# Performance work log

Hardware: AMD Instinct MI355X
Metric: run time of the kernel (lower is better)

The kernel has to match this reference:

```python
import jax, jax.numpy as jnp
import numpy as np

NHEAD = 16
THETA = 10000.0


def _rope_cos_sin(seq_len, head_dim, dtype=jnp.float32):
    # matches precompute_freqs_cis: freqs over even indices, outer with positions
    inv = 1.0 / (THETA ** (jnp.arange(0, head_dim, 2, dtype=jnp.float32) / head_dim))  # [hd/2]
    ang = jnp.arange(seq_len, dtype=jnp.float32)[:, None] * inv[None, :]  # [S, hd/2]
    return jnp.cos(ang).astype(dtype), jnp.sin(ang).astype(dtype)


def _apply_rope(x, cos, sin):
    # x: [B, S, H, D]; pairs (even, odd) treated as complex, multiplied by cis
    B, S, H, D = x.shape
    xr = x.reshape(B, S, H, D // 2, 2)
    a, b = xr[..., 0], xr[..., 1]
    c = cos[None, :, None, :]
    s = sin[None, :, None, :]
    out = jnp.stack([a * c - b * s, a * s + b * c], axis=-1)
    return out.reshape(B, S, H, D)


def setup_inputs() -> dict:
    key = jax.random.key(0)
    ks = jax.random.split(key, 9)
    B, S, D, A = 4, 2048, 1024, 1024
    w = lambda k, i, o: jax.random.normal(k, (i, o), jnp.float32) * 0.02
    return {
        "x": jax.random.normal(ks[0], (B, S, D), jnp.float32),
        "Wq": w(ks[1], D, A), "bq": jnp.zeros((A,), jnp.float32),
        "Wk": w(ks[2], D, A), "bk": jnp.zeros((A,), jnp.float32),
        "Wv": w(ks[3], D, A), "bv": jnp.zeros((A,), jnp.float32),
        "Wo": w(ks[4], A, D), "bo": jnp.zeros((D,), jnp.float32),
    }


def reference(x, Wq, bq, Wk, bk, Wv, bv, Wo, bo):
    B, S, D = x.shape
    A = Wq.shape[1]
    hd = A // NHEAD
    scale = 1.0 / np.sqrt(A / NHEAD)  # 1/dk with dk = sqrt(att_model/nhead)

    Q = (x @ Wq + bq).reshape(B, S, NHEAD, hd)
    K = (x @ Wk + bk).reshape(B, S, NHEAD, hd)
    V = (x @ Wv + bv).reshape(B, S, NHEAD, hd)

    cos, sin = _rope_cos_sin(S, hd)
    Q = _apply_rope(Q, cos, sin)
    K = _apply_rope(K, cos, sin)

    # [B, H, S, S] scores (module materializes this unfused)
    scores = jnp.einsum("bqhd,bkhd->bhqk", Q, K) * scale
    attn = jax.nn.softmax(scores, axis=-1)
    out = jnp.einsum("bhqk,bkhd->bqhd", attn, V).reshape(B, S, A)
    return out @ Wo + bo
```

## Files before the change

### kernel.cpp

```cpp
#include <hip/hip_runtime.h>
#include <math.h>

#define B_N 4
#define S_N 2048
#define D_N 1024
#define H_N 16
#define HD_N 64
#define M_N (B_N * S_N)

typedef __attribute__((ext_vector_type(8))) short bf16x8;
typedef __attribute__((ext_vector_type(4))) float f32x4;

static __device__ __forceinline__ unsigned short f2bf(float f) {
    unsigned int u = __float_as_uint(f);
    u += 0x7FFF + ((u >> 16) & 1);
    return (unsigned short)(u >> 16);
}
static __device__ __forceinline__ float bf2f(unsigned short h) {
    return __uint_as_float(((unsigned int)h) << 16);
}

__global__ __launch_bounds__(256)
void rope_table_kernel(float* __restrict__ cos_t, float* __restrict__ sin_t) {
    int idx = blockIdx.x * 256 + threadIdx.x;
    if (idx >= S_N * 32) return;
    int sp = idx >> 5;
    int p  = idx & 31;
    float inv = powf(10000.0f, -(float)p / 32.0f);
    float ang = (float)sp * inv;
    float s, c;
    sincosf(ang, &s, &c);
    cos_t[idx] = c;
    sin_t[idx] = s;
}

__global__ __launch_bounds__(256)
void splitT_w_kernel(const float* __restrict__ W0, const float* __restrict__ W1,
                     const float* __restrict__ W2, const float* __restrict__ W3,
                     unsigned short* __restrict__ WTh, unsigned short* __restrict__ WTl)
{
    __shared__ float tile[64][65];
    const int k0  = blockIdx.x * 64;
    const int n0  = blockIdx.y * 64;
    const int mat = blockIdx.z;
    const float* __restrict__ W = (mat == 0) ? W0 : (mat == 1) ? W1 : (mat == 2) ? W2 : W3;
    const int t = threadIdx.x;

    #pragma unroll
    for (int p = 0; p < 4; ++p) {
        int idx = t + p * 256;
        int r = idx >> 4, c4 = (idx & 15) * 4;
        float4 v = *(const float4*)&W[(size_t)(k0 + r) * D_N + n0 + c4];
        tile[r][c4]     = v.x;
        tile[r][c4 + 1] = v.y;
        tile[r][c4 + 2] = v.z;
        tile[r][c4 + 3] = v.w;
    }
    __syncthreads();
    #pragma unroll
    for (int p = 0; p < 4; ++p) {
        int idx = t + p * 256;
        int nl = idx >> 4, kc = (idx & 15) * 4;
        ushort4 hi, lo;
        float f0 = tile[kc][nl], f1 = tile[kc + 1][nl];
        float f2 = tile[kc + 2][nl], f3 = tile[kc + 3][nl];
        hi.x = f2bf(f0); lo.x = f2bf(f0 - bf2f(hi.x));
        hi.y = f2bf(f1); lo.y = f2bf(f1 - bf2f(hi.y));
        hi.z = f2bf(f2); lo.z = f2bf(f2 - bf2f(hi.z));
        hi.w = f2bf(f3); lo.w = f2bf(f3 - bf2f(hi.w));
        size_t base = ((size_t)(mat * D_N + n0 + nl)) * D_N + k0 + kc;
        *(ushort4*)&WTh[base] = hi;
        *(ushort4*)&WTl[base] = lo;
    }
}

__device__ __forceinline__ void gemm_core_f32A(
    const float* __restrict__ A,
    const unsigned short* __restrict__ Bh, const unsigned short* __restrict__ Bl,
    int aRow0, int bRow0,
    unsigned short* ldsA, unsigned short* ldsB,
    f32x4 acc[4][4])
{
    const int tid  = threadIdx.x;
    const int wave = tid >> 6;
    const int lane = tid & 63;
    const int l15  = lane & 15;
    const int lg   = lane >> 4;
    const int wr   = wave >> 1;
    const int wc   = wave & 1;

    const float* ga[2];
    int la[2];
    #pragma unroll
    for (int p = 0; p < 2; ++p) {
        int c = tid + p * 256;
        int row = c >> 2, kc = c & 3;
        ga[p] = A + (size_t)(aRow0 + row) * D_N + kc * 8;
        la[p] = row * 72 + kc * 8;
    }
    const unsigned short* gb[4];
    int lb[4];
    #pragma unroll
    for (int p = 0; p < 4; ++p) {
        int c = tid + p * 256;
        int row = c >> 3, ss = c & 7, sel = ss >> 2, kc = ss & 3;
        gb[p] = (sel ? Bl : Bh) + (size_t)(bRow0 + row) * D_N + kc * 8;
        lb[p] = row * 72 + ss * 8;
    }

    for (int kk = 0; kk < D_N / 32; ++kk) {
        float4 av[2][2];
        bf16x8 bv[4];
        #pragma unroll
        for (int p = 0; p < 2; ++p) {
            av[p][0] = *(const float4*)ga[p];
            av[p][1] = *(const float4*)(ga[p] + 4);
            ga[p] += 32;
        }
        #pragma unroll
        for (int p = 0; p < 4; ++p) {
            bv[p] = *(const bf16x8*)gb[p];
            gb[p] += 32;
        }
        __syncthreads();
        #pragma unroll
        for (int p = 0; p < 2; ++p) {
            bf16x8 hi, lo;
            float v[8] = {av[p][0].x, av[p][0].y, av[p][0].z, av[p][0].w,
                          av[p][1].x, av[p][1].y, av[p][1].z, av[p][1].w};
            #pragma unroll
            for (int q = 0; q < 8; ++q) {
                unsigned short h = f2bf(v[q]);
                hi[q] = (short)h;
                lo[q] = (short)f2bf(v[q] - bf2f(h));
            }
            *(bf16x8*)&ldsA[la[p]]      = hi;
            *(bf16x8*)&ldsA[la[p] + 32] = lo;
        }
        #pragma unroll
        for (int p = 0; p < 4; ++p)
            *(bf16x8*)&ldsB[lb[p]] = bv[p];
        __syncthreads();

        bf16x8 ah[4], al[4], bh[4], bl[4];
        #pragma unroll
        for (int i = 0; i < 4; ++i) {
            int ar = wr * 64 + i * 16 + l15;
            ah[i] = *(const bf16x8*)&ldsA[ar * 72 + lg * 8];
            al[i] = *(const bf16x8*)&ldsA[ar * 72 + 32 + lg * 8];
            int br = wc * 64 + i * 16 + l15;
            bh[i] = *(const bf16x8*)&ldsB[br * 72 + lg * 8];
            bl[i] = *(const bf16x8*)&ldsB[br * 72 + 32 + lg * 8];
        }
        #pragma unroll
        for (int i = 0; i < 4; ++i)
            #pragma unroll
            for (int j = 0; j < 4; ++j) {
                acc[i][j] = __builtin_amdgcn_mfma_f32_16x16x32_bf16(ah[i], bh[j], acc[i][j], 0, 0, 0);
                acc[i][j] = __builtin_amdgcn_mfma_f32_16x16x32_bf16(al[i], bh[j], acc[i][j], 0, 0, 0);
                acc[i][j] = __builtin_amdgcn_mfma_f32_16x16x32_bf16(ah[i], bl[j], acc[i][j], 0, 0, 0);
            }
    }
}

__global__ __launch_bounds__(256)
void qkv_gemm_kernel(const float* __restrict__ x,
                     const unsigned short* __restrict__ WTh, const unsigned short* __restrict__ WTl,
                     const float* __restrict__ bq, const float* __restrict__ bk,
                     const float* __restrict__ bv_,
                     const float* __restrict__ cos_t, const float* __restrict__ sin_t,
                     unsigned short* __restrict__ Qh, unsigned short* __restrict__ Ql,
                     unsigned short* __restrict__ Kh, unsigned short* __restrict__ Kl,
                     unsigned short* __restrict__ Vth, unsigned short* __restrict__ Vtl)
{
    __shared__ unsigned short ldsA[128 * 72];
    __shared__ unsigned short ldsB[128 * 72];

    const int m0  = blockIdx.x * 128;
    const int n0  = blockIdx.y * 128;
    const int mat = n0 >> 10;

    f32x4 acc[4][4];
    #pragma unroll
    for (int i = 0; i < 4; ++i)
        #pragma unroll
        for (int j = 0; j < 4; ++j) acc[i][j] = (f32x4){0.f, 0.f, 0.f, 0.f};

    gemm_core_f32A(x, WTh, WTl, m0, n0, ldsA, ldsB, acc);

    const int tid  = threadIdx.x;
    const int wave = tid >> 6;
    const int lane = tid & 63;
    const int l15  = lane & 15;
    const int lg   = lane >> 4;
    const int wr   = wave >> 1;
    const int wc   = wave & 1;

    const float* __restrict__ bias = (mat == 0) ? bq : (mat == 1) ? bk : bv_;
    unsigned short* __restrict__ Hi = (mat == 0) ? Qh : Kh;
    unsigned short* __restrict__ Lo = (mat == 0) ? Ql : Kl;

    #pragma unroll
    for (int i = 0; i < 4; ++i) {
        #pragma unroll
        for (int j = 0; j < 4; ++j) {
            const int nl   = (n0 & 1023) + wc * 64 + j * 16 + l15;
            const int head = nl >> 6;
            const int d    = nl & 63;
            const float bval = bias[nl];
            const int m_base = m0 + wr * 64 + i * 16 + lg * 4;
            const int bb  = m_base >> 11;
            const int sp0 = m_base & (S_N - 1);

            if (mat == 2) {
                ushort4 hi4, lo4;
                float v0 = acc[i][j][0] + bval;
                float v1 = acc[i][j][1] + bval;
                float v2 = acc[i][j][2] + bval;
                float v3 = acc[i][j][3] + bval;
                hi4.x = f2bf(v0); lo4.x = f2bf(v0 - bf2f(hi4.x));
                hi4.y = f2bf(v1); lo4.y = f2bf(v1 - bf2f(hi4.y));
                hi4.z = f2bf(v2); lo4.z = f2bf(v2 - bf2f(hi4.z));
                hi4.w = f2bf(v3); lo4.w = f2bf(v3 - bf2f(hi4.w));
                size_t base = ((size_t)((bb * H_N + head) * HD_N + d)) * S_N + sp0;
                *(ushort4*)&Vth[base] = hi4;
                *(ushort4*)&Vtl[base] = lo4;
            } else {
                const int p = d >> 1;
                const float sgn = (d & 1) ? 1.0f : -1.0f;
                #pragma unroll
                for (int r = 0; r < 4; ++r) {
                    int sp = sp0 + r;
                    float v = acc[i][j][r] + bval;
                    float part = __shfl_xor(v, 1);
                    float c = cos_t[sp * 32 + p];
                    float s = sin_t[sp * 32 + p];
                    float vp = v * c + part * s * sgn;
                    if (mat == 0) vp *= 0.125f;
                    unsigned short hi = f2bf(vp);
                    unsigned short lo = f2bf(vp - bf2f(hi));
                    size_t base = ((size_t)((bb * H_N + head) * S_N + sp)) * HD_N + d;
                    Hi[base] = hi;
                    Lo[base] = lo;
                }
            }
        }
    }
}

__global__ __launch_bounds__(256)
void attn_kernel(const unsigned short* __restrict__ Qh, const unsigned short* __restrict__ Ql,
                 const unsigned short* __restrict__ Kh, const unsigned short* __restrict__ Kl,
                 const unsigned short* __restrict__ Vh, const unsigned short* __restrict__ Vl,
                 float* __restrict__ O)
{
    __shared__ __align__(16) unsigned short KhS[4096];
    __shared__ __align__(16) unsigned short KlS[4096];
    __shared__ __align__(16) unsigned short VhS[4096];
    __shared__ __align__(16) unsigned short VlS[4096];
    __shared__ __align__(16) unsigned short Pb[4][1024];

    const int qt = blockIdx.x;
    const int h  = blockIdx.y;
    const int b  = blockIdx.z;
    const int bh = b * H_N + h;

    const int tid  = threadIdx.x;
    const int wave = tid >> 6;
    const int lane = tid & 63;
    const int l15  = lane & 15;
    const int lg   = lane >> 4;

    const int qrow = qt * 64 + wave * 16 + l15;
    const size_t qbase = ((size_t)bh * S_N + qrow) * HD_N;
    bf16x8 qfh[2], qfl[2];
    qfh[0] = *(const bf16x8*)&Qh[qbase + lg * 8];
    qfh[1] = *(const bf16x8*)&Qh[qbase + 32 + lg * 8];
    qfl[0] = *(const bf16x8*)&Ql[qbase + lg * 8];
    qfl[1] = *(const bf16x8*)&Ql[qbase + 32 + lg * 8];

    f32x4 oacc[4];
    #pragma unroll
    for (int dt = 0; dt < 4; ++dt) oacc[dt] = (f32x4){0.f, 0.f, 0.f, 0.f};
    float m_r[4], l_r[4];
    #pragma unroll
    for (int r = 0; r < 4; ++r) { m_r[r] = -1e30f; l_r[r] = 0.f; }

    for (int kt = 0; kt < S_N / 64; ++kt) {
        __syncthreads();
        #pragma unroll
        for (int t = 0; t < 2; ++t) {
            int c   = tid + t * 256;
            int row = c >> 3;
            int sl  = c & 7;
            int li  = (row * 64 + sl * 8) ^ ((row & 7) << 3);
            size_t gk = ((size_t)bh * S_N + kt * 64 + row) * HD_N + sl * 8;
            size_t gv = ((size_t)bh * HD_N + row) * S_N + kt * 64 + sl * 8;
            bf16x8 vkh = *(const bf16x8*)&Kh[gk];
            bf16x8 vkl = *(const bf16x8*)&Kl[gk];
            bf16x8 vvh = *(const bf16x8*)&Vh[gv];
            bf16x8 vvl = *(const bf16x8*)&Vl[gv];
            *(bf16x8*)&KhS[li] = vkh;
            *(bf16x8*)&KlS[li] = vkl;
            *(bf16x8*)&VhS[li] = vvh;
            *(bf16x8*)&VlS[li] = vvl;
        }
        __syncthreads();

        f32x4 s[4];
        #pragma unroll
        for (int nt = 0; nt < 4; ++nt) s[nt] = (f32x4){0.f, 0.f, 0.f, 0.f};
        #pragma unroll
        for (int ks = 0; ks < 2; ++ks) {
            #pragma unroll
            for (int nt = 0; nt < 4; ++nt) {
                int row = nt * 16 + l15;
                int bi  = (row * 64 + ks * 32 + lg * 8) ^ ((row & 7) << 3);
                bf16x8 fkh = *(const bf16x8*)&KhS[bi];
                bf16x8 fkl = *(const bf16x8*)&KlS[bi];
                s[nt] = __builtin_amdgcn_mfma_f32_16x16x32_bf16(qfh[ks], fkh, s[nt], 0, 0, 0);
                s[nt] = __builtin_amdgcn_mfma_f32_16x16x32_bf16(qfl[ks], fkh, s[nt], 0, 0, 0);
                s[nt] = __builtin_amdgcn_mfma_f32_16x16x32_bf16(qfh[ks], fkl, s[nt], 0, 0, 0);
            }
        }

        #pragma unroll
        for (int r = 0; r < 4; ++r) {
            float mx = fmaxf(fmaxf(s[0][r], s[1][r]), fmaxf(s[2][r], s[3][r]));
            mx = fmaxf(mx, __shfl_xor(mx, 1));
            mx = fmaxf(mx, __shfl_xor(mx, 2));
            mx = fmaxf(mx, __shfl_xor(mx, 4));
            mx = fmaxf(mx, __shfl_xor(mx, 8));
            float mnew = fmaxf(m_r[r], mx);
            float al   = __expf(m_r[r] - mnew);
            float ps   = 0.f;
            #pragma unroll
            for (int nt = 0; nt < 4; ++nt) {
                float p = __expf(s[nt][r] - mnew);
                s[nt][r] = p;
                ps += p;
            }
            ps += __shfl_xor(ps, 1);
            ps += __shfl_xor(ps, 2);
            ps += __shfl_xor(ps, 4);
            ps += __shfl_xor(ps, 8);
            l_r[r] = l_r[r] * al + ps;
            m_r[r] = mnew;
            oacc[0][r] *= al; oacc[1][r] *= al;
            oacc[2][r] *= al; oacc[3][r] *= al;
            int prow = lg * 4 + r;
            #pragma unroll
            for (int nt = 0; nt < 4; ++nt) {
                Pb[wave][(prow * 64 + nt * 16 + l15) ^ ((prow & 7) << 3)] = f2bf(s[nt][r]);
            }
        }
        asm volatile("s_waitcnt lgkmcnt(0)" ::: "memory");

        #pragma unroll
        for (int ks = 0; ks < 2; ++ks) {
            int pi = (l15 * 64 + ks * 32 + lg * 8) ^ ((l15 & 7) << 3);
            bf16x8 pa = *(const bf16x8*)&Pb[wave][pi];
            #pragma unroll
            for (int dt = 0; dt < 4; ++dt) {
                int vrow = dt * 16 + l15;
                int vbi  = (vrow * 64 + ks * 32 + lg * 8) ^ ((vrow & 7) << 3);
                bf16x8 fvh = *(const bf16x8*)&VhS[vbi];
                bf16x8 fvl = *(const bf16x8*)&VlS[vbi];
                oacc[dt] = __builtin_amdgcn_mfma_f32_16x16x32_bf16(pa, fvh, oacc[dt], 0, 0, 0);
                oacc[dt] = __builtin_amdgcn_mfma_f32_16x16x32_bf16(pa, fvl, oacc[dt], 0, 0, 0);
            }
        }
    }

    #pragma unroll
    for (int r = 0; r < 4; ++r) {
        float inv = 1.0f / l_r[r];
        int row = qt * 64 + wave * 16 + lg * 4 + r;
        size_t obase = ((size_t)b * S_N + row) * D_N + h * HD_N;
        #pragma unroll
        for (int dt = 0; dt < 4; ++dt)
            O[obase + dt * 16 + l15] = oacc[dt][r] * inv;
    }
}

__global__ __launch_bounds__(256)
void out_gemm_kernel(const float* __restrict__ A,
                     const unsigned short* __restrict__ WTh, const unsigned short* __restrict__ WTl,
                     const float* __restrict__ bo, float* __restrict__ out)
{
    __shared__ unsigned short ldsA[128 * 72];
    __shared__ unsigned short ldsB[128 * 72];

    const int m0 = blockIdx.x * 128;
    const int n0 = blockIdx.y * 128;

    f32x4 acc[4][4];
    #pragma unroll
    for (int i = 0; i < 4; ++i)
        #pragma unroll
        for (int j = 0; j < 4; ++j) acc[i][j] = (f32x4){0.f, 0.f, 0.f, 0.f};

    gemm_core_f32A(A, WTh, WTl, m0, 3 * D_N + n0, ldsA, ldsB, acc);

    const int tid  = threadIdx.x;
    const int wave = tid >> 6;
    const int lane = tid & 63;
    const int l15  = lane & 15;
    const int lg   = lane >> 4;
    const int wr   = wave >> 1;
    const int wc   = wave & 1;

    #pragma unroll
    for (int i = 0; i < 4; ++i) {
        #pragma unroll
        for (int j = 0; j < 4; ++j) {
            int n = n0 + wc * 64 + j * 16 + l15;
            float bval = bo[n];
            int m_base = m0 + wr * 64 + i * 16 + lg * 4;
            #pragma unroll
            for (int r = 0; r < 4; ++r)
                out[(size_t)(m_base + r) * D_N + n] = acc[i][j][r] + bval;
        }
    }
}

extern "C" void kernel_launch(void* const* d_in, const int* in_sizes, int n_in,
                              void* d_out, int out_size, void* d_ws, size_t ws_size,
                              hipStream_t stream) {
    const float* x  = (const float*)d_in[0];
    const float* Wq = (const float*)d_in[1];
    const float* bq = (const float*)d_in[2];
    const float* Wk = (const float*)d_in[3];
    const float* bk = (const float*)d_in[4];
    const float* Wv = (const float*)d_in[5];
    const float* bv = (const float*)d_in[6];
    const float* Wo = (const float*)d_in[7];
    const float* bo = (const float*)d_in[8];
    float* out = (float*)d_out;

    const size_t NE = (size_t)B_N * H_N * S_N * HD_N;
    const size_t WTE = (size_t)4 * D_N * D_N;

    float* cos_t = (float*)d_ws;
    float* sin_t = cos_t + (size_t)S_N * 32;
    unsigned short* WTh = (unsigned short*)(sin_t + (size_t)S_N * 32);
    unsigned short* WTl = WTh + WTE;
    unsigned short* Qh  = WTl + WTE;
    unsigned short* Ql  = Qh  + NE;
    unsigned short* Kh  = Ql  + NE;
    unsigned short* Kl  = Kh  + NE;
    unsigned short* Vth = Kl  + NE;
    unsigned short* Vtl = Vth + NE;
    float* Obuf = (float*)(Vtl + NE);

    rope_table_kernel<<<256, 256, 0, stream>>>(cos_t, sin_t);

    dim3 gw(16, 16, 4);
    splitT_w_kernel<<<gw, 256, 0, stream>>>(Wq, Wk, Wv, Wo, WTh, WTl);

    dim3 g1(M_N / 128, 24);
    qkv_gemm_kernel<<<g1, 256, 0, stream>>>(x, WTh, WTl, bq, bk, bv,
                                            cos_t, sin_t,
                                            Qh, Ql, Kh, Kl, Vth, Vtl);

    dim3 g2(S_N / 64, H_N, B_N);
    attn_kernel<<<g2, 256, 0, stream>>>(Qh, Ql, Kh, Kl, Vth, Vtl, Obuf);

    dim3 g3(M_N / 128, 8);
    out_gemm_kernel<<<g3, 256, 0, stream>>>(Obuf, WTh, WTl, bo, out);
}
```

Before: 661.6 us.

## Process two query row blocks per wave in attention to reuse K/V tiles

```diff
diff --git a/kernel.cpp b/kernel.cpp
--- a/kernel.cpp
+++ b/kernel.cpp
@@ -258,7 +258,7 @@
     __shared__ __align__(16) unsigned short KlS[4096];
     __shared__ __align__(16) unsigned short VhS[4096];
     __shared__ __align__(16) unsigned short VlS[4096];
-    __shared__ __align__(16) unsigned short Pb[4][1024];
+    __shared__ __align__(16) unsigned short Pb[4][2048];
 
     const int qt = blockIdx.x;
     const int h  = blockIdx.y;
@@ -271,20 +271,26 @@
     const int l15  = lane & 15;
     const int lg   = lane >> 4;
 
-    const int qrow = qt * 64 + wave * 16 + l15;
-    const size_t qbase = ((size_t)bh * S_N + qrow) * HD_N;
-    bf16x8 qfh[2], qfl[2];
-    qfh[0] = *(const bf16x8*)&Qh[qbase + lg * 8];
-    qfh[1] = *(const bf16x8*)&Qh[qbase + 32 + lg * 8];
-    qfl[0] = *(const bf16x8*)&Ql[qbase + lg * 8];
-    qfl[1] = *(const bf16x8*)&Ql[qbase + 32 + lg * 8];
-
-    f32x4 oacc[4];
-    #pragma unroll
-    for (int dt = 0; dt < 4; ++dt) oacc[dt] = (f32x4){0.f, 0.f, 0.f, 0.f};
-    float m_r[4], l_r[4];
-    #pragma unroll
-    for (int r = 0; r < 4; ++r) { m_r[r] = -1e30f; l_r[r] = 0.f; }
+    bf16x8 qfh[2][2], qfl[2][2];
+    #pragma unroll
+    for (int rb = 0; rb < 2; ++rb) {
+        const int qrow = qt * 128 + wave * 32 + rb * 16 + l15;
+        const size_t qbase = ((size_t)bh * S_N + qrow) * HD_N;
+        qfh[rb][0] = *(const bf16x8*)&Qh[qbase + lg * 8];
+        qfh[rb][1] = *(const bf16x8*)&Qh[qbase + 32 + lg * 8];
+        qfl[rb][0] = *(const bf16x8*)&Ql[qbase + lg * 8];
+        qfl[rb][1] = *(const bf16x8*)&Ql[qbase + 32 + lg * 8];
+    }
+
+    f32x4 oacc[2][4];
+    float m_r[2][4], l_r[2][4];
+    #pragma unroll
+    for (int rb = 0; rb < 2; ++rb) {
+        #pragma unroll
+        for (int dt = 0; dt < 4; ++dt) oacc[rb][dt] = (f32x4){0.f, 0.f, 0.f, 0.f};
+        #pragma unroll
+        for (int r = 0; r < 4; ++r) { m_r[rb][r] = -1e30f; l_r[rb][r] = 0.f; }
+    }
 
     for (int kt = 0; kt < S_N / 64; ++kt) {
         __syncthreads();
@@ -307,9 +313,12 @@
         }
         __syncthreads();
 
-        f32x4 s[4];
-        #pragma unroll
-        for (int nt = 0; nt < 4; ++nt) s[nt] = (f32x4){0.f, 0.f, 0.f, 0.f};
+        f32x4 s[2][4];
+        #pragma unroll
+        for (int rb = 0; rb < 2; ++rb)
+            #pragma unroll
+            for (int nt = 0; nt < 4; ++nt) s[rb][nt] = (f32x4){0.f, 0.f, 0.f, 0.f};
+        __builtin_amdgcn_s_setprio(1);
         #pragma unroll
         for (int ks = 0; ks < 2; ++ks) {
             #pragma unroll
@@ -318,68 +327,84 @@
                 int bi  = (row * 64 + ks * 32 + lg * 8) ^ ((row & 7) << 3);
                 bf16x8 fkh = *(const bf16x8*)&KhS[bi];
                 bf16x8 fkl = *(const bf16x8*)&KlS[bi];
-                s[nt] = __builtin_amdgcn_mfma_f32_16x16x32_bf16(qfh[ks], fkh, s[nt], 0, 0, 0);
-                s[nt] = __builtin_amdgcn_mfma_f32_16x16x32_bf16(qfl[ks], fkh, s[nt], 0, 0, 0);
-                s[nt] = __builtin_amdgcn_mfma_f32_16x16x32_bf16(qfh[ks], fkl, s[nt], 0, 0, 0);
-            }
-        }
-
-        #pragma unroll
-        for (int r = 0; r < 4; ++r) {
-            float mx = fmaxf(fmaxf(s[0][r], s[1][r]), fmaxf(s[2][r], s[3][r]));
-            mx = fmaxf(mx, __shfl_xor(mx, 1));
-            mx = fmaxf(mx, __shfl_xor(mx, 2));
-            mx = fmaxf(mx, __shfl_xor(mx, 4));
-            mx = fmaxf(mx, __shfl_xor(mx, 8));
-            float mnew = fmaxf(m_r[r], mx);
-            float al   = __expf(m_r[r] - mnew);
-            float ps   = 0.f;
-            #pragma unroll
-            for (int nt = 0; nt < 4; ++nt) {
-                float p = __expf(s[nt][r] - mnew);
-                s[nt][r] = p;
-                ps += p;
-            }
-            ps += __shfl_xor(ps, 1);
-            ps += __shfl_xor(ps, 2);
-            ps += __shfl_xor(ps, 4);
-            ps += __shfl_xor(ps, 8);
-            l_r[r] = l_r[r] * al + ps;
-            m_r[r] = mnew;
-            oacc[0][r] *= al; oacc[1][r] *= al;
-            oacc[2][r] *= al; oacc[3][r] *= al;
-            int prow = lg * 4 + r;
-            #pragma unroll
-            for (int nt = 0; nt < 4; ++nt) {
-                Pb[wave][(prow * 64 + nt * 16 + l15) ^ ((prow & 7) << 3)] = f2bf(s[nt][r]);
+                #pragma unroll
+                for (int rb = 0; rb < 2; ++rb) {
+                    s[rb][nt] = __builtin_amdgcn_mfma_f32_16x16x32_bf16(qfh[rb][ks], fkh, s[rb][nt], 0, 0, 0);
+                    s[rb][nt] = __builtin_amdgcn_mfma_f32_16x16x32_bf16(qfl[rb][ks], fkh, s[rb][nt], 0, 0, 0);
+                    s[rb][nt] = __builtin_amdgcn_mfma_f32_16x16x32_bf16(qfh[rb][ks], fkl, s[rb][nt], 0, 0, 0);
+                }
+            }
+        }
+        __builtin_amdgcn_s_setprio(0);
+
+        #pragma unroll
+        for (int rb = 0; rb < 2; ++rb) {
+            #pragma unroll
+            for (int r = 0; r < 4; ++r) {
+                float mx = fmaxf(fmaxf(s[rb][0][r], s[rb][1][r]), fmaxf(s[rb][2][r], s[rb][3][r]));
+                mx = fmaxf(mx, __shfl_xor(mx, 1));
+                mx = fmaxf(mx, __shfl_xor(mx, 2));
+                mx = fmaxf(mx, __shfl_xor(mx, 4));
+                mx = fmaxf(mx, __shfl_xor(mx, 8));
+                float mnew = fmaxf(m_r[rb][r], mx);
+                float al   = __expf(m_r[rb][r] - mnew);
+                float ps   = 0.f;
+                #pragma unroll
+                for (int nt = 0; nt < 4; ++nt) {
+                    float p = __expf(s[rb][nt][r] - mnew);
+                    s[rb][nt][r] = p;
+                    ps += p;
+                }
+                ps += __shfl_xor(ps, 1);
+                ps += __shfl_xor(ps, 2);
+                ps += __shfl_xor(ps, 4);
+                ps += __shfl_xor(ps, 8);
+                l_r[rb][r] = l_r[rb][r] * al + ps;
+                m_r[rb][r] = mnew;
+                oacc[rb][0][r] *= al; oacc[rb][1][r] *= al;
+                oacc[rb][2][r] *= al; oacc[rb][3][r] *= al;
+                int prow = rb * 16 + lg * 4 + r;
+                #pragma unroll
+                for (int nt = 0; nt < 4; ++nt) {
+                    Pb[wave][(prow * 64 + nt * 16 + l15) ^ ((prow & 7) << 3)] = f2bf(s[rb][nt][r]);
+                }
             }
         }
         asm volatile("s_waitcnt lgkmcnt(0)" ::: "memory");
 
+        __builtin_amdgcn_s_setprio(1);
         #pragma unroll
         for (int ks = 0; ks < 2; ++ks) {
-            int pi = (l15 * 64 + ks * 32 + lg * 8) ^ ((l15 & 7) << 3);
-            bf16x8 pa = *(const bf16x8*)&Pb[wave][pi];
+            int pr0 = l15;
+            int pr1 = 16 + l15;
+            bf16x8 pa0 = *(const bf16x8*)&Pb[wave][(pr0 * 64 + ks * 32 + lg * 8) ^ ((pr0 & 7) << 3)];
+            bf16x8 pa1 = *(const bf16x8*)&Pb[wave][(pr1 * 64 + ks * 32 + lg * 8) ^ ((pr1 & 7) << 3)];
             #pragma unroll
             for (int dt = 0; dt < 4; ++dt) {
                 int vrow = dt * 16 + l15;
                 int vbi  = (vrow * 64 + ks * 32 + lg * 8) ^ ((vrow & 7) << 3);
                 bf16x8 fvh = *(const bf16x8*)&VhS[vbi];
                 bf16x8 fvl = *(const bf16x8*)&VlS[vbi];
-                oacc[dt] = __builtin_amdgcn_mfma_f32_16x16x32_bf16(pa, fvh, oacc[dt], 0, 0, 0);
-                oacc[dt] = __builtin_amdgcn_mfma_f32_16x16x32_bf16(pa, fvl, oacc[dt], 0, 0, 0);
-            }
-        }
-    }
-
-    #pragma unroll
-    for (int r = 0; r < 4; ++r) {
-        float inv = 1.0f / l_r[r];
-        int row = qt * 64 + wave * 16 + lg * 4 + r;
-        size_t obase = ((size_t)b * S_N + row) * D_N + h * HD_N;
-        #pragma unroll
-        for (int dt = 0; dt < 4; ++dt)
-            O[obase + dt * 16 + l15] = oacc[dt][r] * inv;
+                oacc[0][dt] = __builtin_amdgcn_mfma_f32_16x16x32_bf16(pa0, fvh, oacc[0][dt], 0, 0, 0);
+                oacc[0][dt] = __builtin_amdgcn_mfma_f32_16x16x32_bf16(pa0, fvl, oacc[0][dt], 0, 0, 0);
+                oacc[1][dt] = __builtin_amdgcn_mfma_f32_16x16x32_bf16(pa1, fvh, oacc[1][dt], 0, 0, 0);
+                oacc[1][dt] = __builtin_amdgcn_mfma_f32_16x16x32_bf16(pa1, fvl, oacc[1][dt], 0, 0, 0);
+            }
+        }
+        __builtin_amdgcn_s_setprio(0);
+    }
+
+    #pragma unroll
+    for (int rb = 0; rb < 2; ++rb) {
+        #pragma unroll
+        for (int r = 0; r < 4; ++r) {
+            float inv = 1.0f / l_r[rb][r];
+            int row = qt * 128 + wave * 32 + rb * 16 + lg * 4 + r;
+            size_t obase = ((size_t)b * S_N + row) * D_N + h * HD_N;
+            #pragma unroll
+            for (int dt = 0; dt < 4; ++dt)
+                O[obase + dt * 16 + l15] = oacc[rb][dt][r] * inv;
+        }
     }
 }
 
@@ -463,7 +488,7 @@
                                             cos_t, sin_t,
                                             Qh, Ql, Kh, Kl, Vth, Vtl);
 
-    dim3 g2(S_N / 64, H_N, B_N);
+    dim3 g2(S_N / 128, H_N, B_N);
     attn_kernel<<<g2, 256, 0, stream>>>(Qh, Ql, Kh, Kl, Vth, Vtl, Obuf);
 
     dim3 g3(M_N / 128, 8);
```

Result: faster. 608.1 us (-8.1%).
